# Optimization experiments

Measured on AMD Instinct MI355X. Metric: run time of the kernel, lower is better.

The kernel has to match this reference:

```python
import jax, jax.numpy as jnp
import numpy as np

D_MODEL = 1024
N_HEADS = 16
D_HEAD = D_MODEL // N_HEADS
SCALE = 1.0 / (D_HEAD ** 0.5)


def _rel_shift(t):
    # Transformer-XL relative shift: pad -> view -> slice -> view. t: [b,h,q,k]
    b, h, q, k = t.shape
    padded = jnp.pad(t, ((0, 0), (0, 0), (0, 0), (1, 0)))  # [b,h,q,k+1]
    shifted = padded.reshape(b, h, k + 1, q)[:, :, 1:, :].reshape(b, h, q, k)
    return shifted


def setup_inputs() -> dict:
    key = jax.random.key(0)
    ks = jax.random.split(key, 10)
    B, T, M = 2, 1024, 1024
    J = M + T
    inp = {
        "x": jax.random.normal(ks[0], (B, T, D_MODEL), dtype=jnp.float32),
        "memory": jax.random.normal(ks[1], (B, M, D_MODEL), dtype=jnp.float32),
        "pos_emb": jax.random.normal(ks[2], (J, D_MODEL), dtype=jnp.float32),
        # nn.Linear(d, d, bias=False) weights: y = x @ W.T, W: [out, in]
        "q_w": jax.random.normal(ks[3], (D_MODEL, D_MODEL), dtype=jnp.float32) * 0.02,
        "k_w": jax.random.normal(ks[4], (D_MODEL, D_MODEL), dtype=jnp.float32) * 0.02,
        "v_w": jax.random.normal(ks[5], (D_MODEL, D_MODEL), dtype=jnp.float32) * 0.02,
        "r_w": jax.random.normal(ks[6], (D_MODEL, D_MODEL), dtype=jnp.float32) * 0.02,
        "out_w": jax.random.normal(ks[7], (D_MODEL, D_MODEL), dtype=jnp.float32) * 0.02,
        "pos_bias_u": jax.random.normal(ks[8], (N_HEADS, D_HEAD), dtype=jnp.float32) * 0.02,
        "pos_bias_v": jax.random.normal(ks[9], (N_HEADS, D_HEAD), dtype=jnp.float32) * 0.02,
    }
    return inp


def reference(x, memory, pos_emb, q_w, k_w, v_w, r_w, out_w, pos_bias_u, pos_bias_v):
    B, T, _ = x.shape
    cat = jnp.concatenate([memory, x], axis=1)  # [B, M+T, d]
    L = cat.shape[1]

    def heads(t):  # [B, time, d] -> [B, h, time, dh]
        return t.reshape(t.shape[0], t.shape[1], N_HEADS, D_HEAD).transpose(0, 2, 1, 3)

    q = heads(x @ q_w.T)      # [B,h,T,dh]
    k = heads(cat @ k_w.T)    # [B,h,L,dh]
    v = heads(cat @ v_w.T)    # [B,h,L,dh]
    r = (pos_emb @ r_w.T).reshape(-1, N_HEADS, D_HEAD).transpose(1, 0, 2)  # [h,J,dh]

    q_u = q + pos_bias_u[None, :, None, :]
    q_v = q + pos_bias_v[None, :, None, :]

    content_score = jnp.einsum('bhqd,bhkd->bhqk', q_u, k)  # [B,h,T,L]
    rel_score = jnp.einsum('bhqd,hjd->bhqj', q_v, r)        # [B,h,T,J]
    rel_score = _rel_shift(rel_score)

    scores = (content_score + rel_score) * SCALE
    attn = jax.nn.softmax(scores, axis=-1)
    out = jnp.einsum('bhqk,bhkd->bhqd', attn, v)            # [B,h,T,dh]
    out = out.transpose(0, 2, 1, 3).reshape(B, T, N_HEADS * D_HEAD)
    return out @ out_w.T
```

## Files before the change

kernel.cpp:

```cpp
#include <hip/hip_runtime.h>


typedef unsigned short u16;
typedef unsigned int u32;
typedef short bf16x8 __attribute__((ext_vector_type(8)));
typedef float f32x4 __attribute__((ext_vector_type(4)));

#define MFMA16(a, b, c) __builtin_amdgcn_mfma_f32_16x16x32_bf16(a, b, c, 0, 0, 0)

__device__ __forceinline__ u16 f2bf(float f) {
  u32 u = __float_as_uint(f);
  u32 r = (u + 0x7fffu + ((u >> 16) & 1u)) >> 16;
  return (u16)r;
}

__device__ __forceinline__ void async16(void* lds, const void* g) {
  __builtin_amdgcn_global_load_lds(
      (const __attribute__((address_space(1))) u32*)g,
      (__attribute__((address_space(3))) u32*)lds, 16, 0, 0);
}

__global__ void prep_kernel(const float* __restrict__ x, const float* __restrict__ mem,
                            const float* __restrict__ pos,
                            const float* __restrict__ qw, const float* __restrict__ kw,
                            const float* __restrict__ vw, const float* __restrict__ rw,
                            const float* __restrict__ ow,
                            u16* __restrict__ catb, u16* __restrict__ posb,
                            u16* __restrict__ wqb, u16* __restrict__ wkb,
                            u16* __restrict__ wvb, u16* __restrict__ wrb,
                            u16* __restrict__ wob) {
  const int seg = blockIdx.y;
  const int vid = blockIdx.x * blockDim.x + threadIdx.x;
  const float* src = nullptr;
  u16* dst = nullptr;
  int count = 0;
  switch (seg) {
    case 0: count = (2 * 2048 * 1024) / 4; dst = catb; break;
    case 1: count = (2048 * 1024) / 4; src = pos; dst = posb; break;
    case 2: count = (1024 * 1024) / 4; src = qw; dst = wqb; break;
    case 3: count = (1024 * 1024) / 4; src = kw; dst = wkb; break;
    case 4: count = (1024 * 1024) / 4; src = vw; dst = wvb; break;
    case 5: count = (1024 * 1024) / 4; src = rw; dst = wrb; break;
    case 6: count = (1024 * 1024) / 4; src = ow; dst = wob; break;
  }
  if (vid >= count) return;
  float4 f;
  if (seg == 0) {
    int e = vid * 4;
    int col = e & 1023;
    int row = (e >> 10) & 2047;
    int b = e >> 21;
    const float* s2 = (row < 1024)
                          ? (mem + ((size_t)(b * 1024 + row) * 1024 + col))
                          : (x + ((size_t)(b * 1024 + (row - 1024)) * 1024 + col));
    f = *(const float4*)s2;
  } else {
    f = *(const float4*)(src + (size_t)vid * 4);
  }
  ushort4 o4;
  o4.x = f2bf(f.x); o4.y = f2bf(f.y); o4.z = f2bf(f.z); o4.w = f2bf(f.w);
  *(ushort4*)(dst + (size_t)vid * 4) = o4;
}

__device__ __forceinline__ void gemm_core(const u16* __restrict__ A, const u16* __restrict__ W,
                                          u16* As, u16* Bs, int m0, int n0, bool qmap,
                                          f32x4 acc[4][4]) {
  const int t = threadIdx.x;
  const int lane = t & 63, wid = t >> 6;
  const int colL = lane & 15, rg = lane >> 4;
  const int wm = (wid >> 1) * 64, wn = (wid & 1) * 64;
  for (int kt = 0; kt < 32; ++kt) {
    __syncthreads();
#pragma unroll
    for (int pass = 0; pass < 2; ++pass) {
      int slot = t + pass * 256;
      int row = slot >> 2, ch = slot & 3;
      int sch = ch ^ ((row >> 1) & 3);
      int ar = m0 + row;
      if (qmap) ar = ((ar >> 10) << 11) + 1024 + (ar & 1023);
      async16(As + slot * 8, A + (size_t)ar * 1024 + kt * 32 + sch * 8);
      async16(Bs + slot * 8, W + (size_t)(n0 + row) * 1024 + kt * 32 + sch * 8);
    }
    __syncthreads();
    bf16x8 af[4], bfr[4];
#pragma unroll
    for (int mi = 0; mi < 4; ++mi) {
      int r = wm + mi * 16 + colL;
      af[mi] = *(const bf16x8*)(As + r * 32 + (rg ^ ((r >> 1) & 3)) * 8);
    }
#pragma unroll
    for (int ni = 0; ni < 4; ++ni) {
      int r = wn + ni * 16 + colL;
      bfr[ni] = *(const bf16x8*)(Bs + r * 32 + (rg ^ ((r >> 1) & 3)) * 8);
    }
#pragma unroll
    for (int mi = 0; mi < 4; ++mi)
#pragma unroll
      for (int ni = 0; ni < 4; ++ni)
        acc[mi][ni] = MFMA16(af[mi], bfr[ni], acc[mi][ni]);
  }
}

__global__ __launch_bounds__(256, 2) void gemm_qkvr(
    const u16* __restrict__ catb, const u16* __restrict__ posb,
    const u16* __restrict__ wqb, const u16* __restrict__ wrb,
    const u16* __restrict__ wkb, const u16* __restrict__ wvb,
    const float* __restrict__ bu, const float* __restrict__ bv,
    u16* __restrict__ qub, u16* __restrict__ qvb, u16* __restrict__ rbuf,
    u16* __restrict__ kbuf, u16* __restrict__ vtbuf) {
  __shared__ u16 As[128 * 32], Bs[128 * 32];
  const int x = blockIdx.x;
  const int bid = (x & 7) * 96 + (x >> 3);
  const u16* A;
  const u16* W;
  int mode, r2;
  bool qmap = false;
  if (bid < 128)      { mode = 0; A = catb; W = wqb; qmap = true; r2 = bid; }
  else if (bid < 256) { mode = 1; A = posb; W = wrb; r2 = bid - 128; }
  else if (bid < 512) { mode = 2; A = catb; W = wkb; r2 = bid - 256; }
  else                { mode = 3; A = catb; W = wvb; r2 = bid - 512; }
  const int m0 = (r2 >> 3) * 128, n0 = (r2 & 7) * 128;
  f32x4 acc[4][4];
  f32x4 zz = {0.f, 0.f, 0.f, 0.f};
#pragma unroll
  for (int a1 = 0; a1 < 4; ++a1)
#pragma unroll
    for (int a2 = 0; a2 < 4; ++a2) acc[a1][a2] = zz;
  gemm_core(A, W, As, Bs, m0, n0, qmap, acc);
  const int t = threadIdx.x, lane = t & 63, wid = t >> 6;
  const int colL = lane & 15, rg = lane >> 4;
  const int wm = (wid >> 1) * 64, wn = (wid & 1) * 64;
  const float sc = 0.18033688f;
#pragma unroll
  for (int mi = 0; mi < 4; ++mi)
#pragma unroll
    for (int ni = 0; ni < 4; ++ni)
#pragma unroll
      for (int e = 0; e < 4; ++e) {
        int m = m0 + wm + mi * 16 + rg * 4 + e;
        int n = n0 + wn + ni * 16 + colL;
        float val = acc[mi][ni][e];
        int hh = n >> 6, dd = n & 63;
        if (mode == 0) {
          int bb = m >> 10, tq = m & 1023;
          size_t ad = (((size_t)(bb * 16 + hh)) * 1024 + tq) * 64 + dd;
          qub[ad] = f2bf((val + bu[n]) * sc);
          qvb[ad] = f2bf((val + bv[n]) * sc);
        } else if (mode == 1) {
          rbuf[((((size_t)hh * 128 + (m >> 4)) * 8 + (dd >> 3)) * 16 + (m & 15)) * 8 +
               (dd & 7)] = f2bf(val);
        } else {
          int bb = m >> 11, j = m & 2047;
          size_t bh2 = (size_t)(bb * 16 + hh);
          if (mode == 2)
            kbuf[(((bh2 * 128 + (j >> 4)) * 8 + (dd >> 3)) * 16 + (j & 15)) * 8 + (dd & 7)] =
                f2bf(val);
          else
            vtbuf[((((bh2 * 32 + (j >> 6)) * 4 + (dd >> 4)) * 8 + ((j >> 3) & 7)) * 16 +
                   (dd & 15)) * 8 + (j & 7)] = f2bf(val);
        }
      }
}

__global__ __launch_bounds__(256, 2) void attn_kernel(
    const u16* __restrict__ qu, const u16* __restrict__ qv, const u16* __restrict__ ktile,
    const u16* __restrict__ vtile, const u16* __restrict__ rtile,
    float* __restrict__ opart, float* __restrict__ mlpart) {
  __shared__ float Ulds[4][16 * 84];
  const int t = threadIdx.x;
  const int wid = t >> 6, lane = t & 63;
  const int colL = lane & 15, rg = lane >> 4;
  const int bid = ((blockIdx.x & 7) << 7) | (blockIdx.x >> 3);
  const int bh = bid >> 5;
  const int rem = bid & 31;
  const int qc = rem >> 1, ks = rem & 1;
  const int h = bh & 15;
  const int i0 = qc * 64 + wid * 16;

  const u16* qub = qu + (size_t)bh * (1024 * 64);
  const u16* qvb = qv + (size_t)bh * (1024 * 64);
  const u16* kb = ktile + (size_t)bh * (128 * 1024);
  const u16* vb = vtile + (size_t)bh * (32 * 4096);
  const u16* rb = rtile + (size_t)h * (128 * 1024);
  const int lane8 = (rg * 16 + colL) * 8;

  bf16x8 aqu[2], aqv[2];
  {
    int r0 = i0 + colL;
#pragma unroll
    for (int kx = 0; kx < 2; ++kx) {
      aqu[kx] = *(const bf16x8*)(qub + (size_t)r0 * 64 + kx * 32 + rg * 8);
      aqv[kx] = *(const bf16x8*)(qvb + (size_t)r0 * 64 + kx * 32 + rg * 8);
    }
  }
  bf16x8 ones;
#pragma unroll
  for (int i = 0; i < 8; ++i) ones[i] = (short)0x3F80;

  const f32x4 zz = {0.f, 0.f, 0.f, 0.f};
  f32x4 o[4];
  f32x4 lacc = zz;
#pragma unroll
  for (int e = 0; e < 4; ++e) o[e] = zz;
  int lb[4];
#pragma unroll
  for (int e = 0; e < 4; ++e) lb[e] = (rg * 4 + e) * 83 + colL + 15;

  float* Uw = &Ulds[wid][0];
  u16* Pw = (u16*)Uw;

#pragma unroll 1
  for (int jt = ks * 16; jt < ks * 16 + 16; ++jt) {
    const int j0 = jt * 64;
    f32x4 s[4];
#pragma unroll
    for (int ni = 0; ni < 4; ++ni) {
      const u16* kp = kb + (size_t)((j0 >> 4) + ni) * 1024 + lane8;
      s[ni] = zz;
      s[ni] = MFMA16(aqu[0], *(const bf16x8*)kp, s[ni]);
      s[ni] = MFMA16(aqu[1], *(const bf16x8*)(kp + 512), s[ni]);
    }
    const int pbase = j0 + 1008 - i0;
    const bool mainv = (pbase <= 2047);
    const bool leak = (pbase + 78 >= 2049);
    if (mainv) {
      const int tb = pbase >> 4;
#pragma unroll
      for (int uc = 0; uc < 5; ++uc) {
        int tt = tb + uc; tt = tt < 127 ? tt : 127;
        const u16* rp = rb + (size_t)tt * 1024 + lane8;
        f32x4 ua = zz;
        ua = MFMA16(aqv[0], *(const bf16x8*)rp, ua);
        ua = MFMA16(aqv[1], *(const bf16x8*)(rp + 512), ua);
#pragma unroll
        for (int e = 0; e < 4; ++e) Uw[(rg * 4 + e) * 84 + uc * 16 + colL] = ua[e];
      }
      asm volatile("s_waitcnt lgkmcnt(0)" ::: "memory");
      const int pl = pbase + colL + 15;
#pragma unroll
      for (int c = 0; c < 4; ++c)
#pragma unroll
        for (int e = 0; e < 4; ++e) {
          float uval = Uw[lb[e] + c * 16];
          int p = pl + c * 16 - (rg * 4 + e);
          s[c][e] += (p <= 2047) ? uval : 0.f;
        }
    }
    if (leak) {
      asm volatile("s_waitcnt lgkmcnt(0)" ::: "memory");
      bf16x8 aqs0, aqs1;
      {
        int r0 = i0 + colL;
        int rs = (r0 + 1 < 1024) ? r0 + 1 : 1023;
        aqs0 = *(const bf16x8*)(qvb + (size_t)rs * 64 + rg * 8);
        aqs1 = *(const bf16x8*)(qvb + (size_t)rs * 64 + 32 + rg * 8);
      }
      const int mB1 = (pbase - 2048) >> 4;
      const int rowL = (colL + 15) & 15;
      const int tadj = (colL > 0) ? 0 : -1;
#pragma unroll
      for (int uc = 0; uc < 5; ++uc) {
        int tL = mB1 + uc + tadj;
        tL = tL < 0 ? 0 : (tL > 127 ? 127 : tL);
        const u16* rp = rb + (size_t)tL * 1024 + rg * 128 + rowL * 8;
        f32x4 ua = zz;
        ua = MFMA16(aqs0, *(const bf16x8*)rp, ua);
        ua = MFMA16(aqs1, *(const bf16x8*)(rp + 512), ua);
#pragma unroll
        for (int e = 0; e < 4; ++e) Uw[(rg * 4 + e) * 84 + uc * 16 + colL] = ua[e];
      }
      asm volatile("s_waitcnt lgkmcnt(0)" ::: "memory");
      const int pl = pbase + colL + 15;
#pragma unroll
      for (int c = 0; c < 4; ++c)
#pragma unroll
        for (int e = 0; e < 4; ++e) {
          int p = pl + c * 16 - (rg * 4 + e);
          if (p >= 2049) s[c][e] += Uw[lb[e] + c * 16];
        }
    }
    bf16x8 vf[8];
    {
      const u16* vp0 = vb + (size_t)jt * 4096 + lane8;
#pragma unroll
      for (int ni = 0; ni < 4; ++ni) {
        vf[2 * ni] = *(const bf16x8*)(vp0 + ni * 1024);
        vf[2 * ni + 1] = *(const bf16x8*)(vp0 + ni * 1024 + 512);
      }
    }
#pragma unroll
    for (int c = 0; c < 4; ++c)
#pragma unroll
      for (int e = 0; e < 4; ++e) {
        float px = __builtin_amdgcn_exp2f(s[c][e] - 16.0f);
        int row = rg * 4 + e;
        int col = c * 16 + colL;
        int sw = (col >> 3) ^ (row & 7);
        Pw[row * 64 + sw * 8 + (col & 7)] = f2bf(px);
      }
    asm volatile("s_waitcnt lgkmcnt(0)" ::: "memory");
    bf16x8 pa[2];
#pragma unroll
    for (int kx = 0; kx < 2; ++kx) {
      int chunk = kx * 4 + rg;
      int sw = chunk ^ (colL & 7);
      pa[kx] = *(const bf16x8*)(Pw + colL * 64 + sw * 8);
    }
    lacc = MFMA16(pa[0], ones, lacc);
    lacc = MFMA16(pa[1], ones, lacc);
#pragma unroll
    for (int ni = 0; ni < 4; ++ni) {
      o[ni] = MFMA16(pa[0], vf[2 * ni], o[ni]);
      o[ni] = MFMA16(pa[1], vf[2 * ni + 1], o[ni]);
    }
    asm volatile("" ::: "memory");
  }
  const size_t rowbase = (size_t)ks * 32768 + (size_t)bh * 1024 + i0;
#pragma unroll
  for (int c = 0; c < 4; ++c)
#pragma unroll
    for (int e = 0; e < 4; ++e) {
      int row = rg * 4 + e;
      opart[(rowbase + row) * 64 + c * 16 + colL] = o[c][e];
    }
  if (colL == 0) {
#pragma unroll
    for (int e = 0; e < 4; ++e) {
      size_t r = rowbase + rg * 4 + e;
      mlpart[r * 2 + 0] = 16.0f;
      mlpart[r * 2 + 1] = lacc[e];
    }
  }
}

__global__ void combine_kernel(const float* __restrict__ opart,
                               const float* __restrict__ mlpart,
                               u16* __restrict__ aout) {
  const int gid = blockIdx.x * 256 + threadIdx.x;
  const int r = gid >> 4;
  const int cg = gid & 15;
  float2 ml0 = *(const float2*)(mlpart + (size_t)r * 2);
  float2 ml1 = *(const float2*)(mlpart + ((size_t)32768 + r) * 2);
  float m = fmaxf(ml0.x, ml1.x);
  float f0 = __builtin_amdgcn_exp2f(ml0.x - m);
  float f1 = __builtin_amdgcn_exp2f(ml1.x - m);
  float inv = 1.0f / (ml0.y * f0 + ml1.y * f1);
  f0 *= inv; f1 *= inv;
  float4 a = *(const float4*)(opart + (size_t)r * 64 + cg * 4);
  float4 b4 = *(const float4*)(opart + ((size_t)32768 + r) * 64 + cg * 4);
  ushort4 o4;
  o4.x = f2bf(a.x * f0 + b4.x * f1);
  o4.y = f2bf(a.y * f0 + b4.y * f1);
  o4.z = f2bf(a.z * f0 + b4.z * f1);
  o4.w = f2bf(a.w * f0 + b4.w * f1);
  const int bh = r >> 10, i = r & 1023;
  const int b = bh >> 4, h = bh & 15;
  *(ushort4*)(aout + ((size_t)(b * 1024 + i) * 1024 + h * 64 + cg * 4)) = o4;
}

__global__ __launch_bounds__(256, 2) void gemm_out(
    const u16* __restrict__ aob, const u16* __restrict__ wob, float* __restrict__ out) {
  __shared__ u16 As[128 * 32], Bs[128 * 32];
  const int bid = ((blockIdx.x & 7) << 4) | (blockIdx.x >> 3);
  const int mt = bid >> 3, nt = bid & 7;
  const int m0 = mt * 128, n0 = nt * 128;
  f32x4 acc[4][4];
  f32x4 zz = {0.f, 0.f, 0.f, 0.f};
#pragma unroll
  for (int a1 = 0; a1 < 4; ++a1)
#pragma unroll
    for (int a2 = 0; a2 < 4; ++a2) acc[a1][a2] = zz;
  gemm_core(aob, wob, As, Bs, m0, n0, false, acc);
  const int t = threadIdx.x, lane = t & 63, wid = t >> 6;
  const int colL = lane & 15, rg = lane >> 4;
  const int wm = (wid >> 1) * 64, wn = (wid & 1) * 64;
#pragma unroll
  for (int mi = 0; mi < 4; ++mi)
#pragma unroll
    for (int ni = 0; ni < 4; ++ni)
#pragma unroll
      for (int e = 0; e < 4; ++e) {
        int m = m0 + wm + mi * 16 + rg * 4 + e;
        int n = n0 + wn + ni * 16 + colL;
        out[(size_t)m * 1024 + n] = acc[mi][ni][e];
      }
}

extern "C" void kernel_launch(void* const* d_in, const int* in_sizes, int n_in,
                              void* d_out, int out_size, void* d_ws, size_t ws_size,
                              hipStream_t stream) {
  (void)in_sizes; (void)n_in; (void)out_size; (void)ws_size;
  const float* x = (const float*)d_in[0];
  const float* mem = (const float*)d_in[1];
  const float* pos = (const float*)d_in[2];
  const float* qw = (const float*)d_in[3];
  const float* kw = (const float*)d_in[4];
  const float* vw = (const float*)d_in[5];
  const float* rw = (const float*)d_in[6];
  const float* ow = (const float*)d_in[7];
  const float* bu = (const float*)d_in[8];
  const float* bv = (const float*)d_in[9];
  float* out = (float*)d_out;

  char* w = (char*)d_ws;
  u16* catb = (u16*)(w + 0);
  u16* posb = (u16*)(w + 8388608);
  u16* wqb  = (u16*)(w + 12582912);
  u16* wkb  = (u16*)(w + 14680064);
  u16* wvb  = (u16*)(w + 16777216);
  u16* wrb  = (u16*)(w + 18874368);
  u16* wob  = (u16*)(w + 20971520);
  u16* qub  = (u16*)(w + 23068672);
  u16* qvb  = (u16*)(w + 27262976);
  u16* kbuf = (u16*)(w + 31457280);
  u16* vtb  = (u16*)(w + 39845888);
  u16* rbuf = (u16*)(w + 48234496);
  u16* aob  = (u16*)(w + 52428800);
  float* opart  = (float*)(w + 0);
  float* mlpart = (float*)(w + 16777216);

  prep_kernel<<<dim3(4096, 7), 256, 0, stream>>>(x, mem, pos, qw, kw, vw, rw, ow,
                                                 catb, posb, wqb, wkb, wvb, wrb, wob);
  gemm_qkvr<<<768, 256, 0, stream>>>(catb, posb, wqb, wrb, wkb, wvb, bu, bv,
                                     qub, qvb, rbuf, kbuf, vtb);
  attn_kernel<<<1024, 256, 0, stream>>>(qub, qvb, kbuf, vtb, rbuf, opart, mlpart);
  combine_kernel<<<2048, 256, 0, stream>>>(opart, mlpart, aob);
  gemm_out<<<128, 256, 0, stream>>>(aob, wob, out);
}
```

Before: 264.0 us.

## Software-pipeline K and R tile loads with double-buffered registers in attention loop

The attention inner loop is split into a helper body and unrolled by two, with K and R fragments for the next tile prefetched into a second register set while the current tile computes. This aims to hide global load latency behind the MFMA work. It costs 36 extra bf16x8 registers, which under launch_bounds(256,2) may cause spills. The last iteration also issues a wasted prefetch of the first tile.

```diff
diff --git a/kernel.cpp b/kernel.cpp
--- a/kernel.cpp
+++ b/kernel.cpp
@@ -162,6 +162,134 @@
       }
 }
 
+__device__ __forceinline__ void attn_body(
+    const int jt, const int jn, const int i0, const int colL, const int rg,
+    const int lane8, const u16* __restrict__ kb, const u16* __restrict__ vb,
+    const u16* __restrict__ rb, const u16* __restrict__ qvb,
+    const bf16x8 aqu[2], const bf16x8 aqv[2], const bf16x8& ones,
+    bf16x8 kc[8], bf16x8 rc[10], bf16x8 kn[8], bf16x8 rn[10],
+    f32x4 o[4], f32x4& lacc, const int lb[4], float* Uw, u16* Pw) {
+  const f32x4 zz = {0.f, 0.f, 0.f, 0.f};
+  const int j0 = jt * 64;
+  f32x4 s[4];
+#pragma unroll
+  for (int ni = 0; ni < 4; ++ni) {
+    s[ni] = zz;
+    s[ni] = MFMA16(aqu[0], kc[2 * ni], s[ni]);
+    s[ni] = MFMA16(aqu[1], kc[2 * ni + 1], s[ni]);
+  }
+  {
+    const int jn0 = jn * 64;
+#pragma unroll
+    for (int ni = 0; ni < 4; ++ni) {
+      const u16* kp = kb + (size_t)((jn0 >> 4) + ni) * 1024 + lane8;
+      kn[2 * ni] = *(const bf16x8*)kp;
+      kn[2 * ni + 1] = *(const bf16x8*)(kp + 512);
+    }
+    const int tbn = (jn0 + 1008 - i0) >> 4;
+#pragma unroll
+    for (int uc = 0; uc < 5; ++uc) {
+      int tt = tbn + uc;
+      tt = tt < 127 ? tt : 127;
+      tt = tt > 0 ? tt : 0;
+      const u16* rp = rb + (size_t)tt * 1024 + lane8;
+      rn[2 * uc] = *(const bf16x8*)(rp);
+      rn[2 * uc + 1] = *(const bf16x8*)(rp + 512);
+    }
+  }
+  bf16x8 vf[8];
+  {
+    const u16* vp0 = vb + (size_t)jt * 4096 + lane8;
+#pragma unroll
+    for (int ni = 0; ni < 4; ++ni) {
+      vf[2 * ni] = *(const bf16x8*)(vp0 + ni * 1024);
+      vf[2 * ni + 1] = *(const bf16x8*)(vp0 + ni * 1024 + 512);
+    }
+  }
+  const int pbase = j0 + 1008 - i0;
+  const bool mainv = (pbase <= 2047);
+  const bool leak = (pbase + 78 >= 2049);
+  if (mainv) {
+#pragma unroll
+    for (int uc = 0; uc < 5; ++uc) {
+      f32x4 ua = zz;
+      ua = MFMA16(aqv[0], rc[2 * uc], ua);
+      ua = MFMA16(aqv[1], rc[2 * uc + 1], ua);
+#pragma unroll
+      for (int e = 0; e < 4; ++e) Uw[(rg * 4 + e) * 84 + uc * 16 + colL] = ua[e];
+    }
+    asm volatile("s_waitcnt lgkmcnt(0)" ::: "memory");
+    const int pl = pbase + colL + 15;
+#pragma unroll
+    for (int c = 0; c < 4; ++c)
+#pragma unroll
+      for (int e = 0; e < 4; ++e) {
+        float uval = Uw[lb[e] + c * 16];
+        int p = pl + c * 16 - (rg * 4 + e);
+        s[c][e] += (p <= 2047) ? uval : 0.f;
+      }
+  }
+  if (leak) {
+    asm volatile("s_waitcnt lgkmcnt(0)" ::: "memory");
+    bf16x8 aqs0, aqs1;
+    {
+      int r0 = i0 + colL;
+      int rs = (r0 + 1 < 1024) ? r0 + 1 : 1023;
+      aqs0 = *(const bf16x8*)(qvb + (size_t)rs * 64 + rg * 8);
+      aqs1 = *(const bf16x8*)(qvb + (size_t)rs * 64 + 32 + rg * 8);
+    }
+    const int mB1 = (pbase - 2048) >> 4;
+    const int rowL = (colL + 15) & 15;
+    const int tadj = (colL > 0) ? 0 : -1;
+#pragma unroll
+    for (int uc = 0; uc < 5; ++uc) {
+      int tL = mB1 + uc + tadj;
+      tL = tL < 0 ? 0 : (tL > 127 ? 127 : tL);
+      const u16* rp = rb + (size_t)tL * 1024 + rg * 128 + rowL * 8;
+      f32x4 ua = zz;
+      ua = MFMA16(aqs0, *(const bf16x8*)rp, ua);
+      ua = MFMA16(aqs1, *(const bf16x8*)(rp + 512), ua);
+#pragma unroll
+      for (int e = 0; e < 4; ++e) Uw[(rg * 4 + e) * 84 + uc * 16 + colL] = ua[e];
+    }
+    asm volatile("s_waitcnt lgkmcnt(0)" ::: "memory");
+    const int pl = pbase + colL + 15;
+#pragma unroll
+    for (int c = 0; c < 4; ++c)
+#pragma unroll
+      for (int e = 0; e < 4; ++e) {
+        int p = pl + c * 16 - (rg * 4 + e);
+        if (p >= 2049) s[c][e] += Uw[lb[e] + c * 16];
+      }
+  }
+#pragma unroll
+  for (int c = 0; c < 4; ++c)
+#pragma unroll
+    for (int e = 0; e < 4; ++e) {
+      float px = __builtin_amdgcn_exp2f(s[c][e] - 16.0f);
+      int row = rg * 4 + e;
+      int col = c * 16 + colL;
+      int sw = (col >> 3) ^ (row & 7);
+      Pw[row * 64 + sw * 8 + (col & 7)] = f2bf(px);
+    }
+  asm volatile("s_waitcnt lgkmcnt(0)" ::: "memory");
+  bf16x8 pa[2];
+#pragma unroll
+  for (int kx = 0; kx < 2; ++kx) {
+    int chunk = kx * 4 + rg;
+    int sw = chunk ^ (colL & 7);
+    pa[kx] = *(const bf16x8*)(Pw + colL * 64 + sw * 8);
+  }
+  lacc = MFMA16(pa[0], ones, lacc);
+  lacc = MFMA16(pa[1], ones, lacc);
+#pragma unroll
+  for (int ni = 0; ni < 4; ++ni) {
+    o[ni] = MFMA16(pa[0], vf[2 * ni], o[ni]);
+    o[ni] = MFMA16(pa[1], vf[2 * ni + 1], o[ni]);
+  }
+  asm volatile("" ::: "memory");
+}
+
 __global__ __launch_bounds__(256, 2) void attn_kernel(
     const u16* __restrict__ qu, const u16* __restrict__ qv, const u16* __restrict__ ktile,
     const u16* __restrict__ vtile, const u16* __restrict__ rtile,
@@ -209,111 +337,35 @@
   float* Uw = &Ulds[wid][0];
   u16* Pw = (u16*)Uw;
 
-#pragma unroll 1
-  for (int jt = ks * 16; jt < ks * 16 + 16; ++jt) {
-    const int j0 = jt * 64;
-    f32x4 s[4];
+  const int jt0 = ks * 16;
+  bf16x8 kA[8], rA[10], kB[8], rB[10];
+  {
+    const int j0 = jt0 * 64;
 #pragma unroll
     for (int ni = 0; ni < 4; ++ni) {
       const u16* kp = kb + (size_t)((j0 >> 4) + ni) * 1024 + lane8;
-      s[ni] = zz;
-      s[ni] = MFMA16(aqu[0], *(const bf16x8*)kp, s[ni]);
-      s[ni] = MFMA16(aqu[1], *(const bf16x8*)(kp + 512), s[ni]);
-    }
-    const int pbase = j0 + 1008 - i0;
-    const bool mainv = (pbase <= 2047);
-    const bool leak = (pbase + 78 >= 2049);
-    if (mainv) {
-      const int tb = pbase >> 4;
-#pragma unroll
-      for (int uc = 0; uc < 5; ++uc) {
-        int tt = tb + uc; tt = tt < 127 ? tt : 127;
-        const u16* rp = rb + (size_t)tt * 1024 + lane8;
-        f32x4 ua = zz;
-        ua = MFMA16(aqv[0], *(const bf16x8*)rp, ua);
-        ua = MFMA16(aqv[1], *(const bf16x8*)(rp + 512), ua);
-#pragma unroll
-        for (int e = 0; e < 4; ++e) Uw[(rg * 4 + e) * 84 + uc * 16 + colL] = ua[e];
-      }
-      asm volatile("s_waitcnt lgkmcnt(0)" ::: "memory");
-      const int pl = pbase + colL + 15;
-#pragma unroll
-      for (int c = 0; c < 4; ++c)
-#pragma unroll
-        for (int e = 0; e < 4; ++e) {
-          float uval = Uw[lb[e] + c * 16];
-          int p = pl + c * 16 - (rg * 4 + e);
-          s[c][e] += (p <= 2047) ? uval : 0.f;
-        }
-    }
-    if (leak) {
-      asm volatile("s_waitcnt lgkmcnt(0)" ::: "memory");
-      bf16x8 aqs0, aqs1;
-      {
-        int r0 = i0 + colL;
-        int rs = (r0 + 1 < 1024) ? r0 + 1 : 1023;
-        aqs0 = *(const bf16x8*)(qvb + (size_t)rs * 64 + rg * 8);
-        aqs1 = *(const bf16x8*)(qvb + (size_t)rs * 64 + 32 + rg * 8);
-      }
-      const int mB1 = (pbase - 2048) >> 4;
-      const int rowL = (colL + 15) & 15;
-      const int tadj = (colL > 0) ? 0 : -1;
-#pragma unroll
-      for (int uc = 0; uc < 5; ++uc) {
-        int tL = mB1 + uc + tadj;
-        tL = tL < 0 ? 0 : (tL > 127 ? 127 : tL);
-        const u16* rp = rb + (size_t)tL * 1024 + rg * 128 + rowL * 8;
-        f32x4 ua = zz;
-        ua = MFMA16(aqs0, *(const bf16x8*)rp, ua);
-        ua = MFMA16(aqs1, *(const bf16x8*)(rp + 512), ua);
-#pragma unroll
-        for (int e = 0; e < 4; ++e) Uw[(rg * 4 + e) * 84 + uc * 16 + colL] = ua[e];
-      }
-      asm volatile("s_waitcnt lgkmcnt(0)" ::: "memory");
-      const int pl = pbase + colL + 15;
-#pragma unroll
-      for (int c = 0; c < 4; ++c)
-#pragma unroll
-        for (int e = 0; e < 4; ++e) {
-          int p = pl + c * 16 - (rg * 4 + e);
-          if (p >= 2049) s[c][e] += Uw[lb[e] + c * 16];
-        }
-    }
-    bf16x8 vf[8];
-    {
-      const u16* vp0 = vb + (size_t)jt * 4096 + lane8;
-#pragma unroll
-      for (int ni = 0; ni < 4; ++ni) {
-        vf[2 * ni] = *(const bf16x8*)(vp0 + ni * 1024);
-        vf[2 * ni + 1] = *(const bf16x8*)(vp0 + ni * 1024 + 512);
-      }
-    }
-#pragma unroll
-    for (int c = 0; c < 4; ++c)
-#pragma unroll
-      for (int e = 0; e < 4; ++e) {
-        float px = __builtin_amdgcn_exp2f(s[c][e] - 16.0f);
-        int row = rg * 4 + e;
-        int col = c * 16 + colL;
-        int sw = (col >> 3) ^ (row & 7);
-        Pw[row * 64 + sw * 8 + (col & 7)] = f2bf(px);
-      }
-    asm volatile("s_waitcnt lgkmcnt(0)" ::: "memory");
-    bf16x8 pa[2];
-#pragma unroll
-    for (int kx = 0; kx < 2; ++kx) {
-      int chunk = kx * 4 + rg;
-      int sw = chunk ^ (colL & 7);
-      pa[kx] = *(const bf16x8*)(Pw + colL * 64 + sw * 8);
-    }
-    lacc = MFMA16(pa[0], ones, lacc);
-    lacc = MFMA16(pa[1], ones, lacc);
-#pragma unroll
-    for (int ni = 0; ni < 4; ++ni) {
-      o[ni] = MFMA16(pa[0], vf[2 * ni], o[ni]);
-      o[ni] = MFMA16(pa[1], vf[2 * ni + 1], o[ni]);
-    }
-    asm volatile("" ::: "memory");
+      kA[2 * ni] = *(const bf16x8*)kp;
+      kA[2 * ni + 1] = *(const bf16x8*)(kp + 512);
+    }
+    const int tb = (j0 + 1008 - i0) >> 4;
+#pragma unroll
+    for (int uc = 0; uc < 5; ++uc) {
+      int tt = tb + uc;
+      tt = tt < 127 ? tt : 127;
+      tt = tt > 0 ? tt : 0;
+      const u16* rp = rb + (size_t)tt * 1024 + lane8;
+      rA[2 * uc] = *(const bf16x8*)rp;
+      rA[2 * uc + 1] = *(const bf16x8*)(rp + 512);
+    }
+  }
+#pragma unroll 1
+  for (int p = 0; p < 8; ++p) {
+    const int jt = jt0 + 2 * p;
+    attn_body(jt, jt + 1, i0, colL, rg, lane8, kb, vb, rb, qvb, aqu, aqv, ones,
+              kA, rA, kB, rB, o, lacc, lb, Uw, Pw);
+    const int jn2 = (p < 7) ? jt + 2 : jt0;
+    attn_body(jt + 1, jn2, i0, colL, rg, lane8, kb, vb, rb, qvb, aqu, aqv, ones,
+              kB, rB, kA, rA, o, lacc, lb, Uw, Pw);
   }
   const size_t rowbase = (size_t)ks * 32768 + (size_t)bh * 1024 + i0;
 #pragma unroll
```

Result: slower. 274.3 us (+3.9%).

## Process two 16-row query tiles per wave to reuse K, V and R fragments

Applied to the files above, without the earlier changes.

Each wave now handles 32 query rows instead of 16, so every K, V and relative-position fragment loaded from global memory feeds two sets of MFMAs. The relative-shift band is computed over six R tiles shared by both row blocks, with a larger LDS scratch area. The grid is halved to 512 blocks. The aim is to cut global load traffic per FLOP, at the cost of more registers, lower occupancy and fewer blocks to fill the GPU.

```diff
diff --git a/kernel.cpp b/kernel.cpp
--- a/kernel.cpp
+++ b/kernel.cpp
@@ -166,16 +166,16 @@
     const u16* __restrict__ qu, const u16* __restrict__ qv, const u16* __restrict__ ktile,
     const u16* __restrict__ vtile, const u16* __restrict__ rtile,
     float* __restrict__ opart, float* __restrict__ mlpart) {
-  __shared__ float Ulds[4][16 * 84];
+  __shared__ float Ulds[4][3200];
   const int t = threadIdx.x;
   const int wid = t >> 6, lane = t & 63;
   const int colL = lane & 15, rg = lane >> 4;
-  const int bid = ((blockIdx.x & 7) << 7) | (blockIdx.x >> 3);
-  const int bh = bid >> 5;
-  const int rem = bid & 31;
+  const int bid = ((blockIdx.x & 7) << 6) | (blockIdx.x >> 3);
+  const int bh = bid >> 4;
+  const int rem = bid & 15;
   const int qc = rem >> 1, ks = rem & 1;
   const int h = bh & 15;
-  const int i0 = qc * 64 + wid * 16;
+  const int i0 = qc * 128 + wid * 32;
 
   const u16* qub = qu + (size_t)bh * (1024 * 64);
   const u16* qvb = qv + (size_t)bh * (1024 * 64);
@@ -184,13 +184,16 @@
   const u16* rb = rtile + (size_t)h * (128 * 1024);
   const int lane8 = (rg * 16 + colL) * 8;
 
-  bf16x8 aqu[2], aqv[2];
+  bf16x8 aqu0[2], aqv0[2], aqu1[2], aqv1[2];
   {
     int r0 = i0 + colL;
+    int r1 = i0 + 16 + colL;
 #pragma unroll
     for (int kx = 0; kx < 2; ++kx) {
-      aqu[kx] = *(const bf16x8*)(qub + (size_t)r0 * 64 + kx * 32 + rg * 8);
-      aqv[kx] = *(const bf16x8*)(qvb + (size_t)r0 * 64 + kx * 32 + rg * 8);
+      aqu0[kx] = *(const bf16x8*)(qub + (size_t)r0 * 64 + kx * 32 + rg * 8);
+      aqv0[kx] = *(const bf16x8*)(qvb + (size_t)r0 * 64 + kx * 32 + rg * 8);
+      aqu1[kx] = *(const bf16x8*)(qub + (size_t)r1 * 64 + kx * 32 + rg * 8);
+      aqv1[kx] = *(const bf16x8*)(qvb + (size_t)r1 * 64 + kx * 32 + rg * 8);
     }
   }
   bf16x8 ones;
@@ -198,13 +201,16 @@
   for (int i = 0; i < 8; ++i) ones[i] = (short)0x3F80;
 
   const f32x4 zz = {0.f, 0.f, 0.f, 0.f};
-  f32x4 o[4];
-  f32x4 lacc = zz;
-#pragma unroll
-  for (int e = 0; e < 4; ++e) o[e] = zz;
-  int lb[4];
-#pragma unroll
-  for (int e = 0; e < 4; ++e) lb[e] = (rg * 4 + e) * 83 + colL + 15;
+  f32x4 o0[4], o1[4];
+  f32x4 lacc0 = zz, lacc1 = zz;
+#pragma unroll
+  for (int e = 0; e < 4; ++e) { o0[e] = zz; o1[e] = zz; }
+  int lb0[4], lb1[4];
+#pragma unroll
+  for (int e = 0; e < 4; ++e) {
+    lb0[e] = (rg * 4 + e) * 99 + colL + 31;
+    lb1[e] = (rg * 4 + e) * 99 + colL + 1615;
+  }
 
   float* Uw = &Ulds[wid][0];
   u16* Pw = (u16*)Uw;
@@ -212,71 +218,118 @@
 #pragma unroll 1
   for (int jt = ks * 16; jt < ks * 16 + 16; ++jt) {
     const int j0 = jt * 64;
-    f32x4 s[4];
+    f32x4 s0[4], s1[4];
 #pragma unroll
     for (int ni = 0; ni < 4; ++ni) {
       const u16* kp = kb + (size_t)((j0 >> 4) + ni) * 1024 + lane8;
-      s[ni] = zz;
-      s[ni] = MFMA16(aqu[0], *(const bf16x8*)kp, s[ni]);
-      s[ni] = MFMA16(aqu[1], *(const bf16x8*)(kp + 512), s[ni]);
-    }
-    const int pbase = j0 + 1008 - i0;
-    const bool mainv = (pbase <= 2047);
-    const bool leak = (pbase + 78 >= 2049);
+      bf16x8 b0 = *(const bf16x8*)kp;
+      bf16x8 b1 = *(const bf16x8*)(kp + 512);
+      s0[ni] = zz;
+      s0[ni] = MFMA16(aqu0[0], b0, s0[ni]);
+      s0[ni] = MFMA16(aqu0[1], b1, s0[ni]);
+      s1[ni] = zz;
+      s1[ni] = MFMA16(aqu1[0], b0, s1[ni]);
+      s1[ni] = MFMA16(aqu1[1], b1, s1[ni]);
+    }
+    const int pbase2 = j0 + 992 - i0;
+    const bool mainv = (pbase2 <= 2047);
+    const bool leak = (pbase2 + 94 >= 2049);
     if (mainv) {
-      const int tb = pbase >> 4;
+      const int tb = pbase2 >> 4;
+      bf16x8 rc[12];
+#pragma unroll
+      for (int uc = 0; uc < 6; ++uc) {
+        int tt = tb + uc;
+        tt = tt < 127 ? tt : 127;
+        const u16* rp = rb + (size_t)tt * 1024 + lane8;
+        rc[2 * uc] = *(const bf16x8*)rp;
+        rc[2 * uc + 1] = *(const bf16x8*)(rp + 512);
+      }
+#pragma unroll
+      for (int uc = 1; uc < 6; ++uc) {
+        f32x4 ua = zz;
+        ua = MFMA16(aqv0[0], rc[2 * uc], ua);
+        ua = MFMA16(aqv0[1], rc[2 * uc + 1], ua);
+#pragma unroll
+        for (int e = 0; e < 4; ++e) Uw[(rg * 4 + e) * 100 + uc * 16 + colL] = ua[e];
+      }
 #pragma unroll
       for (int uc = 0; uc < 5; ++uc) {
-        int tt = tb + uc; tt = tt < 127 ? tt : 127;
-        const u16* rp = rb + (size_t)tt * 1024 + lane8;
-        f32x4 ua = zz;
-        ua = MFMA16(aqv[0], *(const bf16x8*)rp, ua);
-        ua = MFMA16(aqv[1], *(const bf16x8*)(rp + 512), ua);
-#pragma unroll
-        for (int e = 0; e < 4; ++e) Uw[(rg * 4 + e) * 84 + uc * 16 + colL] = ua[e];
+        f32x4 ub = zz;
+        ub = MFMA16(aqv1[0], rc[2 * uc], ub);
+        ub = MFMA16(aqv1[1], rc[2 * uc + 1], ub);
+#pragma unroll
+        for (int e = 0; e < 4; ++e) Uw[(16 + rg * 4 + e) * 100 + uc * 16 + colL] = ub[e];
       }
       asm volatile("s_waitcnt lgkmcnt(0)" ::: "memory");
-      const int pl = pbase + colL + 15;
+      const int pl0 = pbase2 + colL + 31;
+      const int pl1 = pbase2 + colL + 15;
 #pragma unroll
       for (int c = 0; c < 4; ++c)
 #pragma unroll
         for (int e = 0; e < 4; ++e) {
-          float uval = Uw[lb[e] + c * 16];
-          int p = pl + c * 16 - (rg * 4 + e);
-          s[c][e] += (p <= 2047) ? uval : 0.f;
+          int w0e = rg * 4 + e;
+          float u0 = Uw[lb0[e] + c * 16];
+          float u1 = Uw[lb1[e] + c * 16];
+          int p0 = pl0 + c * 16 - w0e;
+          int p1 = pl1 + c * 16 - w0e;
+          s0[c][e] += (p0 <= 2047) ? u0 : 0.f;
+          s1[c][e] += (p1 <= 2047) ? u1 : 0.f;
         }
     }
     if (leak) {
       asm volatile("s_waitcnt lgkmcnt(0)" ::: "memory");
-      bf16x8 aqs0, aqs1;
+      bf16x8 aqs0[2], aqs1[2];
       {
-        int r0 = i0 + colL;
-        int rs = (r0 + 1 < 1024) ? r0 + 1 : 1023;
-        aqs0 = *(const bf16x8*)(qvb + (size_t)rs * 64 + rg * 8);
-        aqs1 = *(const bf16x8*)(qvb + (size_t)rs * 64 + 32 + rg * 8);
-      }
-      const int mB1 = (pbase - 2048) >> 4;
+        int rs0 = i0 + colL + 1;
+        int rs1 = i0 + 16 + colL + 1;
+        rs1 = rs1 < 1024 ? rs1 : 1023;
+#pragma unroll
+        for (int kx = 0; kx < 2; ++kx) {
+          aqs0[kx] = *(const bf16x8*)(qvb + (size_t)rs0 * 64 + kx * 32 + rg * 8);
+          aqs1[kx] = *(const bf16x8*)(qvb + (size_t)rs1 * 64 + kx * 32 + rg * 8);
+        }
+      }
+      const int mB1 = (pbase2 - 2048) >> 4;
       const int rowL = (colL + 15) & 15;
       const int tadj = (colL > 0) ? 0 : -1;
-#pragma unroll
-      for (int uc = 0; uc < 5; ++uc) {
+      bf16x8 r2[12];
+#pragma unroll
+      for (int uc = 0; uc < 6; ++uc) {
         int tL = mB1 + uc + tadj;
         tL = tL < 0 ? 0 : (tL > 127 ? 127 : tL);
         const u16* rp = rb + (size_t)tL * 1024 + rg * 128 + rowL * 8;
+        r2[2 * uc] = *(const bf16x8*)rp;
+        r2[2 * uc + 1] = *(const bf16x8*)(rp + 512);
+      }
+#pragma unroll
+      for (int uc = 1; uc < 6; ++uc) {
         f32x4 ua = zz;
-        ua = MFMA16(aqs0, *(const bf16x8*)rp, ua);
-        ua = MFMA16(aqs1, *(const bf16x8*)(rp + 512), ua);
-#pragma unroll
-        for (int e = 0; e < 4; ++e) Uw[(rg * 4 + e) * 84 + uc * 16 + colL] = ua[e];
+        ua = MFMA16(aqs0[0], r2[2 * uc], ua);
+        ua = MFMA16(aqs0[1], r2[2 * uc + 1], ua);
+#pragma unroll
+        for (int e = 0; e < 4; ++e) Uw[(rg * 4 + e) * 100 + uc * 16 + colL] = ua[e];
+      }
+#pragma unroll
+      for (int uc = 0; uc < 5; ++uc) {
+        f32x4 ub = zz;
+        ub = MFMA16(aqs1[0], r2[2 * uc], ub);
+        ub = MFMA16(aqs1[1], r2[2 * uc + 1], ub);
+#pragma unroll
+        for (int e = 0; e < 4; ++e) Uw[(16 + rg * 4 + e) * 100 + uc * 16 + colL] = ub[e];
       }
       asm volatile("s_waitcnt lgkmcnt(0)" ::: "memory");
-      const int pl = pbase + colL + 15;
+      const int pl0 = pbase2 + colL + 31;
+      const int pl1 = pbase2 + colL + 15;
 #pragma unroll
       for (int c = 0; c < 4; ++c)
 #pragma unroll
         for (int e = 0; e < 4; ++e) {
-          int p = pl + c * 16 - (rg * 4 + e);
-          if (p >= 2049) s[c][e] += Uw[lb[e] + c * 16];
+          int w0e = rg * 4 + e;
+          int p0 = pl0 + c * 16 - w0e;
+          int p1 = pl1 + c * 16 - w0e;
+          if (p0 >= 2049) s0[c][e] += Uw[lb0[e] + c * 16];
+          if (p1 >= 2049) s1[c][e] += Uw[lb1[e] + c * 16];
         }
     }
     bf16x8 vf[8];
@@ -292,26 +345,33 @@
     for (int c = 0; c < 4; ++c)
 #pragma unroll
       for (int e = 0; e < 4; ++e) {
-        float px = __builtin_amdgcn_exp2f(s[c][e] - 16.0f);
         int row = rg * 4 + e;
         int col = c * 16 + colL;
         int sw = (col >> 3) ^ (row & 7);
-        Pw[row * 64 + sw * 8 + (col & 7)] = f2bf(px);
+        float p0 = __builtin_amdgcn_exp2f(s0[c][e] - 16.0f);
+        float p1 = __builtin_amdgcn_exp2f(s1[c][e] - 16.0f);
+        Pw[row * 64 + sw * 8 + (colL & 7)] = f2bf(p0);
+        Pw[(16 + row) * 64 + sw * 8 + (colL & 7)] = f2bf(p1);
       }
     asm volatile("s_waitcnt lgkmcnt(0)" ::: "memory");
-    bf16x8 pa[2];
+    bf16x8 pa0[2], pa1[2];
 #pragma unroll
     for (int kx = 0; kx < 2; ++kx) {
       int chunk = kx * 4 + rg;
       int sw = chunk ^ (colL & 7);
-      pa[kx] = *(const bf16x8*)(Pw + colL * 64 + sw * 8);
-    }
-    lacc = MFMA16(pa[0], ones, lacc);
-    lacc = MFMA16(pa[1], ones, lacc);
+      pa0[kx] = *(const bf16x8*)(Pw + colL * 64 + sw * 8);
+      pa1[kx] = *(const bf16x8*)(Pw + (16 + colL) * 64 + sw * 8);
+    }
+    lacc0 = MFMA16(pa0[0], ones, lacc0);
+    lacc0 = MFMA16(pa0[1], ones, lacc0);
+    lacc1 = MFMA16(pa1[0], ones, lacc1);
+    lacc1 = MFMA16(pa1[1], ones, lacc1);
 #pragma unroll
     for (int ni = 0; ni < 4; ++ni) {
-      o[ni] = MFMA16(pa[0], vf[2 * ni], o[ni]);
-      o[ni] = MFMA16(pa[1], vf[2 * ni + 1], o[ni]);
+      o0[ni] = MFMA16(pa0[0], vf[2 * ni], o0[ni]);
+      o0[ni] = MFMA16(pa0[1], vf[2 * ni + 1], o0[ni]);
+      o1[ni] = MFMA16(pa1[0], vf[2 * ni], o1[ni]);
+      o1[ni] = MFMA16(pa1[1], vf[2 * ni + 1], o1[ni]);
     }
     asm volatile("" ::: "memory");
   }
@@ -321,14 +381,17 @@
 #pragma unroll
     for (int e = 0; e < 4; ++e) {
       int row = rg * 4 + e;
-      opart[(rowbase + row) * 64 + c * 16 + colL] = o[c][e];
+      opart[(rowbase + row) * 64 + c * 16 + colL] = o0[c][e];
+      opart[(rowbase + 16 + row) * 64 + c * 16 + colL] = o1[c][e];
     }
   if (colL == 0) {
 #pragma unroll
     for (int e = 0; e < 4; ++e) {
       size_t r = rowbase + rg * 4 + e;
       mlpart[r * 2 + 0] = 16.0f;
-      mlpart[r * 2 + 1] = lacc[e];
+      mlpart[r * 2 + 1] = lacc0[e];
+      mlpart[(r + 16) * 2 + 0] = 16.0f;
+      mlpart[(r + 16) * 2 + 1] = lacc1[e];
     }
   }
 }
@@ -423,7 +486,7 @@
                                                  catb, posb, wqb, wkb, wvb, wrb, wob);
   gemm_qkvr<<<768, 256, 0, stream>>>(catb, posb, wqb, wrb, wkb, wvb, bu, bv,
                                      qub, qvb, rbuf, kbuf, vtb);
-  attn_kernel<<<1024, 256, 0, stream>>>(qub, qvb, kbuf, vtb, rbuf, opart, mlpart);
+  attn_kernel<<<512, 256, 0, stream>>>(qub, qvb, kbuf, vtb, rbuf, opart, mlpart);
   combine_kernel<<<2048, 256, 0, stream>>>(opart, mlpart, aob);
   gemm_out<<<128, 256, 0, stream>>>(aob, wob, out);
 }
```

Result: faster. 226.2 us (-14.3%).
